# Optimization experiments

Measured on AMD Instinct MI355X. Metric: run time of the kernel, lower is better.

The kernel has to match this reference:

```python
import jax, jax.numpy as jnp
import numpy as np

EPS = 1e-5
B, L, DM, DI, DR, DS, K = 1, 1024, 2048, 4096, 128, 16, 3
DT_MAX, DT_MIN, DT_FLOOR = 0.1, 0.001, 1e-4


def setup_inputs() -> dict:
    key = jax.random.key(0)
    ks = jax.random.split(key, 10)
    sc = lambda k, sh, s=0.02: (jax.random.normal(k, sh, jnp.float32) * s)
    # dt_proj bias init (softplus-inverse of dt sampled log-uniform in [dt_min, dt_max])
    dt = jnp.exp(jax.random.uniform(ks[7], (DI,), jnp.float32)
                 * (np.log(DT_MAX) - np.log(DT_MIN)) + np.log(DT_MIN))
    dt = jnp.clip(dt, DT_FLOOR, None)
    inv_dt = dt + jnp.log(-jnp.expm1(-dt))
    dt_std = DR ** (-0.5)  # dt_rank**-0.5 * dt_scale
    return {
        "x": jax.random.normal(ks[0], (B, L, DM), jnp.float32),
        "h": jnp.zeros((B, L, DI, DS), jnp.float32),
        "norm_w": jnp.ones((DM,), jnp.float32),
        "in_proj_w": sc(ks[1], (2 * DI, DM)),
        "conv_w": sc(ks[2], (DI, 1, K), 0.1),      # depthwise: (out=DI, in/groups=1, K)
        "conv_b": jnp.zeros((DI,), jnp.float32),
        "x_proj_w": sc(ks[3], (DR + 2 * DS, DI)),
        "dt_proj_w": jax.random.uniform(ks[4], (DI, DR), jnp.float32, -dt_std, dt_std),
        "dt_proj_b": inv_dt,
        "A_log": jnp.log(jnp.tile(jnp.arange(1, DS + 1, dtype=jnp.float32), (DI, 1))),
        "D": jnp.ones((DI,), jnp.float32),
        "out_proj_w": sc(ks[5], (DM, DI)),
    }


def reference(x, h, norm_w, in_proj_w, conv_w, conv_b, x_proj_w,
              dt_proj_w, dt_proj_b, A_log, D, out_proj_w):
    # RMSNorm
    xn = x * jax.lax.rsqrt(jnp.mean(x * x, axis=-1, keepdims=True) + EPS) * norm_w
    # in_proj -> split into x-branch and gate z
    xz = xn @ in_proj_w.T                      # (B,L,2*DI)
    xs, z = xz[..., :DI], xz[..., DI:]
    # depthwise conv over sequence (padding preserves L for odd K)
    xc = jax.lax.conv_general_dilated(
        jnp.transpose(xs, (0, 2, 1)), conv_w, (1,), [((K - 1) // 2, (K - 1) // 2)],
        dimension_numbers=("NCH", "OIH", "NCH"), feature_group_count=DI)
    xc = jnp.transpose(xc, (0, 2, 1)) + conv_b  # (B,L,DI)
    xc = jax.nn.silu(xc)
    # ssm_step (elementwise over L; h is per-position state)
    A = -jnp.exp(A_log)                        # (DI,DS)
    dBC = xc @ x_proj_w.T                      # (B,L,DR+2*DS)
    delta = jax.nn.softplus(dBC[..., :DR] @ dt_proj_w.T + dt_proj_b)  # (B,L,DI)
    Bm = dBC[..., DR:DR + DS]                  # (B,L,DS)
    Cm = dBC[..., DR + DS:]                    # (B,L,DS)
    deltaA = jnp.exp(delta[..., None] * A)     # (B,L,DI,DS)
    BX = delta[..., None] * Bm[:, :, None, :] * xc[..., None]  # (B,L,DI,DS)
    h_new = deltaA * h + BX                    # (B,L,DI,DS)
    y = jnp.einsum("blds,bls->bld", h_new, Cm) + D * xc
    out = (y * jax.nn.silu(z)) @ out_proj_w.T + xn  # residual adds normed x
    return out, h_new
```

## Files before the change

### kernel.cpp

```cpp
#include <hip/hip_runtime.h>
#include <hip/hip_bf16.h>
#include <math.h>

#define L_   1024
#define DM_  2048
#define DI_  4096
#define DR_  128
#define DS_  16
#define DBC_ 160

typedef __attribute__((ext_vector_type(4))) float f32x4;
typedef __attribute__((ext_vector_type(8))) short s16x8;

__device__ inline unsigned short f2b(float f) {
  unsigned int u = __float_as_uint(f);
  u += 0x7fffu + ((u >> 16) & 1u);
  return (unsigned short)(u >> 16);
}
__device__ inline float b2f(unsigned short u) {
  return __uint_as_float(((unsigned int)u) << 16);
}

__device__ inline void gload_lds16(const void* g, void* l) {
  __builtin_amdgcn_global_load_lds(
      (const __attribute__((address_space(1))) void*)g,
      (__attribute__((address_space(3))) void*)l, 16, 0, 0);
}

__launch_bounds__(256)
__global__ void rms_convert_kernel(const float* __restrict__ x, const float* __restrict__ w,
                                   unsigned short* __restrict__ xnb,
                                   const float* __restrict__ w_in, const float* __restrict__ w_out,
                                   const float* __restrict__ w_dt, const float* __restrict__ w_xp,
                                   unsigned short* __restrict__ wib, unsigned short* __restrict__ wob,
                                   unsigned short* __restrict__ dtwb, unsigned short* __restrict__ xpwb) {
  if (blockIdx.x < L_) {
    int l = blockIdx.x;
    const float4* xr = (const float4*)(x + (size_t)l * DM_);
    const float4* wr = (const float4*)w;
    float4 v0 = xr[threadIdx.x];
    float4 v1 = xr[threadIdx.x + 256];
    float ss = v0.x*v0.x + v0.y*v0.y + v0.z*v0.z + v0.w*v0.w
             + v1.x*v1.x + v1.y*v1.y + v1.z*v1.z + v1.w*v1.w;
    for (int off = 32; off > 0; off >>= 1) ss += __shfl_down(ss, off, 64);
    __shared__ float sbuf[4];
    int lane = threadIdx.x & 63, wid = threadIdx.x >> 6;
    if (lane == 0) sbuf[wid] = ss;
    __syncthreads();
    float tot = sbuf[0] + sbuf[1] + sbuf[2] + sbuf[3];
    float scale = rsqrtf(tot / (float)DM_ + 1e-5f);
    float4 w0 = wr[threadIdx.x], w1 = wr[threadIdx.x + 256];
    float4 o0, o1;
    o0.x = v0.x * scale * w0.x; o0.y = v0.y * scale * w0.y;
    o0.z = v0.z * scale * w0.z; o0.w = v0.w * scale * w0.w;
    o1.x = v1.x * scale * w1.x; o1.y = v1.y * scale * w1.y;
    o1.z = v1.z * scale * w1.z; o1.w = v1.w * scale * w1.w;
    uint2 p0, p1;
    p0.x = (unsigned)f2b(o0.x) | ((unsigned)f2b(o0.y) << 16);
    p0.y = (unsigned)f2b(o0.z) | ((unsigned)f2b(o0.w) << 16);
    p1.x = (unsigned)f2b(o1.x) | ((unsigned)f2b(o1.y) << 16);
    p1.y = (unsigned)f2b(o1.z) | ((unsigned)f2b(o1.w) << 16);
    uint2* ob = (uint2*)(xnb + (size_t)l * DM_);
    ob[threadIdx.x] = p0;
    ob[threadIdx.x + 256] = p1;
    return;
  }
  const int N1 = 2 * DI_ * DM_ / 4;
  const int N2 = DM_ * DI_ / 4;
  const int N3 = DI_ * DR_ / 4;
  const int N4 = DBC_ * DI_ / 4;
  int i = (blockIdx.x - L_) * 256 + threadIdx.x;
  const float* src; unsigned short* dst; int off;
  if (i < N1)                { src = w_in;  dst = wib;  off = i; }
  else if (i < N1 + N2)      { src = w_out; dst = wob;  off = i - N1; }
  else if (i < N1 + N2 + N3) { src = w_dt;  dst = dtwb; off = i - N1 - N2; }
  else if (i < N1 + N2 + N3 + N4) { src = w_xp; dst = xpwb; off = i - N1 - N2 - N3; }
  else return;
  float4 v = ((const float4*)src)[off];
  uint2 p;
  p.x = (unsigned)f2b(v.x) | ((unsigned)f2b(v.y) << 16);
  p.y = (unsigned)f2b(v.z) | ((unsigned)f2b(v.w) << 16);
  ((uint2*)dst)[off] = p;
}

template<int EPI>
__launch_bounds__(256)
__global__ void gemm_bf16_mfma(const unsigned short* __restrict__ A,
                               const unsigned short* __restrict__ W,
                               void* __restrict__ Cv_, int M, int N, int K,
                               const float* __restrict__ aux) {
  __shared__ unsigned short As[2][128 * 32];
  __shared__ unsigned short Ws[2][128 * 32];
  int nwg = gridDim.x * gridDim.y;
  int flat = blockIdx.y * gridDim.x + blockIdx.x;
  int q8 = nwg >> 3;
  int swz = (flat & 7) * q8 + (flat >> 3);
  int bxi = swz % gridDim.x, byi = swz / gridDim.x;
  int bm = byi * 128, bn = bxi * 128;
  int tid = threadIdx.x;
  int w = tid >> 6, lane = tid & 63;
  int wr = (w >> 1) * 64, wc = (w & 1) * 64;
  int ch0 = w * 64 + lane, ch1 = (4 + w) * 64 + lane;
  int row0 = ch0 >> 2, kc0 = ch0 & 3;
  int row1 = ch1 >> 2, kc1 = ch1 & 3;

  f32x4 acc[4][4];
#pragma unroll
  for (int m = 0; m < 4; m++)
#pragma unroll
    for (int n = 0; n < 4; n++) acc[m][n] = (f32x4){0.f, 0.f, 0.f, 0.f};

  int kb = lane >> 4, r = lane & 15;

#define STAGE_(buf, k0)                                                          \
  do {                                                                           \
    gload_lds16(A + (size_t)(bm + row0) * K + (k0) + kc0 * 8, &As[buf][ch0 * 8]);\
    gload_lds16(W + (size_t)(bn + row0) * K + (k0) + kc0 * 8, &Ws[buf][ch0 * 8]);\
    gload_lds16(A + (size_t)(bm + row1) * K + (k0) + kc1 * 8, &As[buf][ch1 * 8]);\
    gload_lds16(W + (size_t)(bn + row1) * K + (k0) + kc1 * 8, &Ws[buf][ch1 * 8]);\
  } while (0)

  STAGE_(0, 0);
  __syncthreads();
  int nt = K >> 5;
  for (int t = 0; t < nt; t++) {
    int cur = t & 1;
    if (t + 1 < nt) STAGE_(cur ^ 1, (t + 1) * 32);
    s16x8 a[4], b[4];
#pragma unroll
    for (int m = 0; m < 4; m++)
      a[m] = *(const s16x8*)(&As[cur][(wr + m * 16 + r) * 32 + kb * 8]);
#pragma unroll
    for (int n = 0; n < 4; n++)
      b[n] = *(const s16x8*)(&Ws[cur][(wc + n * 16 + r) * 32 + kb * 8]);
#pragma unroll
    for (int m = 0; m < 4; m++)
#pragma unroll
      for (int n = 0; n < 4; n++)
        acc[m][n] = __builtin_amdgcn_mfma_f32_16x16x32_bf16(a[m], b[n], acc[m][n], 0, 0, 0);
    __syncthreads();
  }
#undef STAGE_
  int q = lane >> 4;
#pragma unroll
  for (int m = 0; m < 4; m++) {
#pragma unroll
    for (int n = 0; n < 4; n++) {
#pragma unroll
      for (int j = 0; j < 4; j++) {
        int row = bm + wr + m * 16 + q * 4 + j;
        int col = bn + wc + n * 16 + r;
        float v = acc[m][n][j];
        if (EPI == 1) {
          v += aux[col];
          v = fmaxf(v, 0.f) + log1pf(__expf(-fabsf(v)));
          ((unsigned short*)Cv_)[(size_t)row * N + col] = f2b(v);
        }
        if (EPI == 3) {
          ((unsigned short*)Cv_)[(size_t)row * N + col] = f2b(v);
        }
      }
    }
  }
}

__launch_bounds__(256)
__global__ void gemm_bf16_mfma_bm64(const unsigned short* __restrict__ A,
                                    const unsigned short* __restrict__ W,
                                    float* __restrict__ C, int M, int N, int K,
                                    const unsigned short* __restrict__ auxb) {
  __shared__ unsigned short As[2][64 * 32];
  __shared__ unsigned short Ws[2][128 * 32];
  int nwg = gridDim.x * gridDim.y;
  int flat = blockIdx.y * gridDim.x + blockIdx.x;
  int q8 = nwg >> 3;
  int swz = (flat & 7) * q8 + (flat >> 3);
  int bxi = swz % gridDim.x, byi = swz / gridDim.x;
  int bm = byi * 64, bn = bxi * 128;
  int tid = threadIdx.x;
  int w = tid >> 6, lane = tid & 63;
  int wr = (w >> 1) * 32, wc = (w & 1) * 64;
  int chA = w * 64 + lane;
  int rowA = chA >> 2, kcA = chA & 3;
  int ch0 = w * 64 + lane, ch1 = (4 + w) * 64 + lane;
  int row0 = ch0 >> 2, kc0 = ch0 & 3;
  int row1 = ch1 >> 2, kc1 = ch1 & 3;
  f32x4 acc[2][4];
#pragma unroll
  for (int m = 0; m < 2; m++)
#pragma unroll
    for (int n = 0; n < 4; n++) acc[m][n] = (f32x4){0.f, 0.f, 0.f, 0.f};

  int kb = lane >> 4, r = lane & 15;

#define STAGE_(buf, k0)                                                          \
  do {                                                                           \
    gload_lds16(A + (size_t)(bm + rowA) * K + (k0) + kcA * 8, &As[buf][chA * 8]);\
    gload_lds16(W + (size_t)(bn + row0) * K + (k0) + kc0 * 8, &Ws[buf][ch0 * 8]);\
    gload_lds16(W + (size_t)(bn + row1) * K + (k0) + kc1 * 8, &Ws[buf][ch1 * 8]);\
  } while (0)

  STAGE_(0, 0);
  __syncthreads();
  int nt = K >> 5;
  for (int t = 0; t < nt; t++) {
    int cur = t & 1;
    if (t + 1 < nt) STAGE_(cur ^ 1, (t + 1) * 32);
    s16x8 a[2], b[4];
#pragma unroll
    for (int m = 0; m < 2; m++)
      a[m] = *(const s16x8*)(&As[cur][(wr + m * 16 + r) * 32 + kb * 8]);
#pragma unroll
    for (int n = 0; n < 4; n++)
      b[n] = *(const s16x8*)(&Ws[cur][(wc + n * 16 + r) * 32 + kb * 8]);
#pragma unroll
    for (int m = 0; m < 2; m++)
#pragma unroll
      for (int n = 0; n < 4; n++)
        acc[m][n] = __builtin_amdgcn_mfma_f32_16x16x32_bf16(a[m], b[n], acc[m][n], 0, 0, 0);
    __syncthreads();
  }
#undef STAGE_
  int q = lane >> 4;
#pragma unroll
  for (int m = 0; m < 2; m++) {
#pragma unroll
    for (int n = 0; n < 4; n++) {
#pragma unroll
      for (int j = 0; j < 4; j++) {
        int row = bm + wr + m * 16 + q * 4 + j;
        int col = bn + wc + n * 16 + r;
        C[(size_t)row * N + col] = acc[m][n][j] + b2f(auxb[(size_t)row * N + col]);
      }
    }
  }
}

__launch_bounds__(256)
__global__ void conv_silu_kernel(const unsigned short* __restrict__ xzb, const float* __restrict__ cw,
                                 const float* __restrict__ cb, unsigned short* __restrict__ xcb) {
  int i8 = (blockIdx.x * 256 + threadIdx.x) * 8;
  int l = i8 >> 12, d0 = i8 & (DI_ - 1);
  const unsigned short* base = xzb + (size_t)l * (2 * DI_) + d0;
  s16x8 vm = {}, vp = {};
  s16x8 v0 = *(const s16x8*)base;
  if (l > 0)      vm = *(const s16x8*)(base - 2 * DI_);
  if (l < L_ - 1) vp = *(const s16x8*)(base + 2 * DI_);
  float wv[24];
#pragma unroll
  for (int j = 0; j < 6; j++) *(float4*)&wv[j * 4] = *(const float4*)&cw[d0 * 3 + j * 4];
  float bv[8];
  *(float4*)&bv[0] = *(const float4*)&cb[d0];
  *(float4*)&bv[4] = *(const float4*)&cb[d0 + 4];
  unsigned short outv[8];
#pragma unroll
  for (int j = 0; j < 8; j++) {
    float acc = bv[j];
    acc = fmaf(wv[j * 3 + 0], b2f(((const unsigned short*)&vm)[j]), acc);
    acc = fmaf(wv[j * 3 + 1], b2f(((const unsigned short*)&v0)[j]), acc);
    acc = fmaf(wv[j * 3 + 2], b2f(((const unsigned short*)&vp)[j]), acc);
    float sig = 1.f / (1.f + __expf(-acc));
    outv[j] = f2b(acc * sig);
  }
  *(s16x8*)(xcb + i8) = *(s16x8*)outv;
}

__launch_bounds__(256)
__global__ void xproj_stage1_mfma(const unsigned short* __restrict__ xcb,
                                  const unsigned short* __restrict__ Wb,
                                  float* __restrict__ part) {
  __shared__ unsigned short As[2][64 * 32];
  __shared__ unsigned short Bs[2][160 * 32];
  int sp = blockIdx.x;
  int l0 = blockIdx.y * 64;
  int tid = threadIdx.x, w = tid >> 6, lane = tid & 63;
  int wr = (w >> 1) * 32, wc = (w & 1) * 80;
  int kb = lane >> 4, r = lane & 15;
  int chA = w * 64 + lane;
  int rowA = chA >> 2, kcA = chA & 3;
  f32x4 acc[2][5];
#pragma unroll
  for (int m = 0; m < 2; m++)
#pragma unroll
    for (int n = 0; n < 5; n++) acc[m][n] = (f32x4){0.f, 0.f, 0.f, 0.f};

#define STAGE_(buf, k0)                                                            \
  do {                                                                             \
    gload_lds16(xcb + (size_t)(l0 + rowA) * DI_ + (k0) + kcA * 8, &As[buf][chA * 8]);\
    _Pragma("unroll")                                                              \
    for (int i = 0; i < 3; i++) {                                                  \
      int g = i * 4 + w;                                                           \
      if (g < 10) {                                                                \
        int ch = g * 64 + lane;                                                    \
        int row = ch >> 2, kc = ch & 3;                                            \
        gload_lds16(Wb + (size_t)row * DI_ + (k0) + kc * 8, &Bs[buf][ch * 8]);     \
      }                                                                            \
    }                                                                              \
  } while (0)

  int kbase = sp * 256;
  STAGE_(0, kbase);
  __syncthreads();
  for (int kt = 0; kt < 8; kt++) {
    int cur = kt & 1;
    if (kt + 1 < 8) STAGE_(cur ^ 1, kbase + (kt + 1) * 32);
    s16x8 a[2], b[5];
#pragma unroll
    for (int m = 0; m < 2; m++)
      a[m] = *(const s16x8*)(&As[cur][(wr + m * 16 + r) * 32 + kb * 8]);
#pragma unroll
    for (int n = 0; n < 5; n++)
      b[n] = *(const s16x8*)(&Bs[cur][(wc + n * 16 + r) * 32 + kb * 8]);
#pragma unroll
    for (int m = 0; m < 2; m++)
#pragma unroll
      for (int n = 0; n < 5; n++)
        acc[m][n] = __builtin_amdgcn_mfma_f32_16x16x32_bf16(a[m], b[n], acc[m][n], 0, 0, 0);
    __syncthreads();
  }
#undef STAGE_
  int q = lane >> 4;
  float* pb = part + (size_t)sp * (L_ * DBC_) + (size_t)l0 * DBC_;
#pragma unroll
  for (int m = 0; m < 2; m++)
#pragma unroll
    for (int n = 0; n < 5; n++)
#pragma unroll
      for (int j = 0; j < 4; j++)
        pb[(size_t)(wr + m * 16 + q * 4 + j) * DBC_ + wc + n * 16 + r] = acc[m][n][j];
}

__launch_bounds__(256)
__global__ void xproj_stage2(const float* __restrict__ part, float* __restrict__ dBC,
                             unsigned short* __restrict__ dtb) {
  int i = blockIdx.x * 256 + threadIdx.x;
  float s = 0.f;
#pragma unroll
  for (int sp = 0; sp < 16; sp++) s += part[(size_t)sp * (L_ * DBC_) + i];
  dBC[i] = s;
  int l = i / DBC_, col = i - l * DBC_;
  if (col < DR_) dtb[(size_t)l * DR_ + col] = f2b(s);
}

__launch_bounds__(256)
__global__ void ssm_kernel2(const unsigned short* __restrict__ xzb, const unsigned short* __restrict__ xcb,
                            const float* __restrict__ dBC, const unsigned short* __restrict__ deltab,
                            const float* __restrict__ h, const float* __restrict__ A_log,
                            const float* __restrict__ Dp, float* __restrict__ h_out,
                            unsigned short* __restrict__ yzb) {
  int pair = threadIdx.x >> 2;
  int q = threadIdx.x & 3;
  for (int base = blockIdx.x * 64; base < L_ * DI_; base += gridDim.x * 64) {
    int idx = base + pair;
    int l = idx >> 12, d = idx & (DI_ - 1);
    float dv = b2f(deltab[idx]);
    float xv = b2f(xcb[idx]);
    float4 hv = *(const float4*)(h + (size_t)idx * DS_ + q * 4);
    float4 Al = *(const float4*)(A_log + (size_t)d * DS_ + q * 4);
    float4 Bv = *(const float4*)(dBC + (size_t)l * DBC_ + DR_ + q * 4);
    float4 Cv = *(const float4*)(dBC + (size_t)l * DBC_ + DR_ + DS_ + q * 4);
    float4 hn;
    hn.x = __expf(dv * -__expf(Al.x)) * hv.x + dv * Bv.x * xv;
    hn.y = __expf(dv * -__expf(Al.y)) * hv.y + dv * Bv.y * xv;
    hn.z = __expf(dv * -__expf(Al.z)) * hv.z + dv * Bv.z * xv;
    hn.w = __expf(dv * -__expf(Al.w)) * hv.w + dv * Bv.w * xv;
    *(float4*)(h_out + (size_t)idx * DS_ + q * 4) = hn;
    float y = hn.x * Cv.x + hn.y * Cv.y + hn.z * Cv.z + hn.w * Cv.w;
    y += __shfl_xor(y, 1, 64);
    y += __shfl_xor(y, 2, 64);
    if (q == 0) {
      y = fmaf(Dp[d], xv, y);
      float zv = b2f(xzb[(size_t)l * (2 * DI_) + DI_ + d]);
      float sig = 1.f / (1.f + __expf(-zv));
      yzb[idx] = f2b(y * zv * sig);
    }
  }
}

extern "C" void kernel_launch(void* const* d_in, const int* in_sizes, int n_in,
                              void* d_out, int out_size, void* d_ws, size_t ws_size,
                              hipStream_t stream) {
  const float* x         = (const float*)d_in[0];
  const float* h         = (const float*)d_in[1];
  const float* norm_w    = (const float*)d_in[2];
  const float* in_proj_w = (const float*)d_in[3];
  const float* conv_w    = (const float*)d_in[4];
  const float* conv_b    = (const float*)d_in[5];
  const float* x_proj_w  = (const float*)d_in[6];
  const float* dt_proj_w = (const float*)d_in[7];
  const float* dt_proj_b = (const float*)d_in[8];
  const float* A_log     = (const float*)d_in[9];
  const float* Dvec      = (const float*)d_in[10];
  const float* out_projw = (const float*)d_in[11];

  float* out   = (float*)d_out;
  float* h_out = out + (size_t)L_ * DM_;

  float* ws    = (float*)d_ws;
  float* dBC   = ws;
  float* part  = dBC   + (size_t)L_ * DBC_;
  unsigned short* xnb   = (unsigned short*)(part + (size_t)16 * L_ * DBC_);
  unsigned short* wib   = xnb   + (size_t)L_ * DM_;
  unsigned short* wob   = wib   + (size_t)2 * DI_ * DM_;
  unsigned short* yzb   = wob   + (size_t)DM_ * DI_;
  unsigned short* dtb   = yzb   + (size_t)L_ * DI_;
  unsigned short* dtwb  = dtb   + (size_t)L_ * DR_;
  unsigned short* xpwb  = dtwb  + (size_t)DI_ * DR_;
  unsigned short* xcb   = xpwb  + (size_t)DBC_ * DI_;
  unsigned short* xzb   = xcb   + (size_t)L_ * DI_;
  unsigned short* deltab= xzb   + (size_t)L_ * 2 * DI_;

  const int CONV_BLKS = (2 * DI_ * DM_ + DM_ * DI_ + DI_ * DR_ + DBC_ * DI_) / 4 / 256;
  rms_convert_kernel<<<L_ + CONV_BLKS, 256, 0, stream>>>(
      x, norm_w, xnb, in_proj_w, out_projw, dt_proj_w, x_proj_w, wib, wob, dtwb, xpwb);
  gemm_bf16_mfma<3><<<dim3(2 * DI_ / 128, L_ / 128), 256, 0, stream>>>(
      xnb, wib, xzb, L_, 2 * DI_, DM_, nullptr);
  conv_silu_kernel<<<L_ * DI_ / 8 / 256, 256, 0, stream>>>(xzb, conv_w, conv_b, xcb);
  xproj_stage1_mfma<<<dim3(16, 16), 256, 0, stream>>>(xcb, xpwb, part);
  xproj_stage2<<<L_ * DBC_ / 256, 256, 0, stream>>>(part, dBC, dtb);
  gemm_bf16_mfma<1><<<dim3(DI_ / 128, L_ / 128), 256, 0, stream>>>(
      dtb, dtwb, deltab, L_, DI_, DR_, dt_proj_b);
  ssm_kernel2<<<4096, 256, 0, stream>>>(
      xzb, xcb, dBC, deltab, h, A_log, Dvec, h_out, yzb);
  gemm_bf16_mfma_bm64<<<dim3(DM_ / 128, L_ / 64), 256, 0, stream>>>(
      yzb, wob, out, L_, DM_, DI_, xnb);
}
```

Measured before the change: 314.8 us.

## Triple-buffer GEMM LDS staging with partial vmcnt waits

Both bf16 MFMA GEMM kernels move from double to triple buffering of the A/W tiles in LDS, prefetching two k-steps ahead. The full __syncthreads at the end of each step is replaced by an s_waitcnt vmcnt(N) that waits only for the older stage, followed by a raw s_barrier. This lets global-to-LDS loads stay in flight across an iteration so load latency is hidden. In exchange, LDS use per block rises by half, which may lower occupancy. The hand-coded vmcnt counts must also match the number of loads issued per stage.

```diff
diff --git a/kernel.cpp b/kernel.cpp
--- a/kernel.cpp
+++ b/kernel.cpp
@@ -89,8 +89,8 @@
                                const unsigned short* __restrict__ W,
                                void* __restrict__ Cv_, int M, int N, int K,
                                const float* __restrict__ aux) {
-  __shared__ unsigned short As[2][128 * 32];
-  __shared__ unsigned short Ws[2][128 * 32];
+  __shared__ unsigned short As[3][128 * 32];
+  __shared__ unsigned short Ws[3][128 * 32];
   int nwg = gridDim.x * gridDim.y;
   int flat = blockIdx.y * gridDim.x + blockIdx.x;
   int q8 = nwg >> 3;
@@ -120,12 +120,17 @@
     gload_lds16(W + (size_t)(bn + row1) * K + (k0) + kc1 * 8, &Ws[buf][ch1 * 8]);\
   } while (0)
 
+  int nt = K >> 5;
   STAGE_(0, 0);
-  __syncthreads();
-  int nt = K >> 5;
+  STAGE_(1, 32);
+  asm volatile("s_waitcnt vmcnt(4)" ::: "memory");
+  __builtin_amdgcn_s_barrier();
+  int cur = 0;
   for (int t = 0; t < nt; t++) {
-    int cur = t & 1;
-    if (t + 1 < nt) STAGE_(cur ^ 1, (t + 1) * 32);
+    if (t + 2 < nt) {
+      int nxt = cur + 2; if (nxt >= 3) nxt -= 3;
+      STAGE_(nxt, (t + 2) * 32);
+    }
     s16x8 a[4], b[4];
 #pragma unroll
     for (int m = 0; m < 4; m++)
@@ -138,7 +143,10 @@
 #pragma unroll
       for (int n = 0; n < 4; n++)
         acc[m][n] = __builtin_amdgcn_mfma_f32_16x16x32_bf16(a[m], b[n], acc[m][n], 0, 0, 0);
-    __syncthreads();
+    if (t + 2 < nt) asm volatile("s_waitcnt vmcnt(4)" ::: "memory");
+    else            asm volatile("s_waitcnt vmcnt(0)" ::: "memory");
+    __builtin_amdgcn_s_barrier();
+    cur = (cur + 1 == 3) ? 0 : cur + 1;
   }
 #undef STAGE_
   int q = lane >> 4;
@@ -169,8 +177,8 @@
                                     const unsigned short* __restrict__ W,
                                     float* __restrict__ C, int M, int N, int K,
                                     const unsigned short* __restrict__ auxb) {
-  __shared__ unsigned short As[2][64 * 32];
-  __shared__ unsigned short Ws[2][128 * 32];
+  __shared__ unsigned short As[3][64 * 32];
+  __shared__ unsigned short Ws[3][128 * 32];
   int nwg = gridDim.x * gridDim.y;
   int flat = blockIdx.y * gridDim.x + blockIdx.x;
   int q8 = nwg >> 3;
@@ -200,12 +208,17 @@
     gload_lds16(W + (size_t)(bn + row1) * K + (k0) + kc1 * 8, &Ws[buf][ch1 * 8]);\
   } while (0)
 
+  int nt = K >> 5;
   STAGE_(0, 0);
-  __syncthreads();
-  int nt = K >> 5;
+  STAGE_(1, 32);
+  asm volatile("s_waitcnt vmcnt(3)" ::: "memory");
+  __builtin_amdgcn_s_barrier();
+  int cur = 0;
   for (int t = 0; t < nt; t++) {
-    int cur = t & 1;
-    if (t + 1 < nt) STAGE_(cur ^ 1, (t + 1) * 32);
+    if (t + 2 < nt) {
+      int nxt = cur + 2; if (nxt >= 3) nxt -= 3;
+      STAGE_(nxt, (t + 2) * 32);
+    }
     s16x8 a[2], b[4];
 #pragma unroll
     for (int m = 0; m < 2; m++)
@@ -218,7 +231,10 @@
 #pragma unroll
       for (int n = 0; n < 4; n++)
         acc[m][n] = __builtin_amdgcn_mfma_f32_16x16x32_bf16(a[m], b[n], acc[m][n], 0, 0, 0);
-    __syncthreads();
+    if (t + 2 < nt) asm volatile("s_waitcnt vmcnt(3)" ::: "memory");
+    else            asm volatile("s_waitcnt vmcnt(0)" ::: "memory");
+    __builtin_amdgcn_s_barrier();
+    cur = (cur + 1 == 3) ? 0 : cur + 1;
   }
 #undef STAGE_
   int q = lane >> 4;
```

Measured after the change: 325.6 us. 1.03x slower.
